# Kernel optimization log

Measured on AMD Instinct MI355X. Metric: run time of the kernel, lower is better.

The kernel has to match this reference:

```python
import jax, jax.numpy as jnp
import numpy as np

N_HEAD, D_MODEL, D_K, D_V = 16, 1024, 64, 64
B, S = 2, 2048
LN_EPS = 1e-5


def setup_inputs() -> dict:
    key = jax.random.key(0)
    ks = jax.random.split(key, 9)
    std_qk = np.sqrt(2.0 / (D_MODEL + D_K)).astype(np.float32)
    std_v = np.sqrt(2.0 / (D_MODEL + D_V)).astype(np.float32)
    return {
        "q": jax.random.normal(ks[0], (B, S, D_MODEL), jnp.float32),
        "k": jax.random.normal(ks[1], (B, S, D_MODEL), jnp.float32),
        "v": jax.random.normal(ks[2], (B, S, D_MODEL), jnp.float32),
        # nn.Linear weights stored as [out, in]; we apply x @ W.T
        "w_qs": jax.random.normal(ks[3], (N_HEAD * D_K, D_MODEL), jnp.float32) * std_qk,
        "w_ks": jax.random.normal(ks[4], (N_HEAD * D_K, D_MODEL), jnp.float32) * std_qk,
        "w_vs": jax.random.normal(ks[5], (N_HEAD * D_V, D_MODEL), jnp.float32) * std_v,
        "fc_w": jax.random.normal(ks[6], (D_MODEL, N_HEAD * D_V), jnp.float32) * np.sqrt(2.0 / (D_MODEL + N_HEAD * D_V)).astype(np.float32),
        "fc_b": jnp.zeros((D_MODEL,), jnp.float32),
        "ln_g": jnp.ones((D_MODEL,), jnp.float32),
        "ln_b": jnp.zeros((D_MODEL,), jnp.float32),
    }


def reference(q, k, v, w_qs, w_ks, w_vs, fc_w, fc_b, ln_g, ln_b):
    temperature = jnp.asarray(np.power(D_K, 0.5), q.dtype)
    residual = q
    # projections -> [b, s, h, d]
    qh = (q @ w_qs.T).reshape(B, S, N_HEAD, D_K)
    kh = (k @ w_ks.T).reshape(B, S, N_HEAD, D_K)
    vh = (v @ w_vs.T).reshape(B, S, N_HEAD, D_V)
    # scaled dot-product attention (dropout = identity in eval)
    attn = jnp.einsum('bqhd,bkhd->bhqk', qh, kh) / temperature
    attn = jax.nn.softmax(attn, axis=-1)  # (log_softmax in source is unused)
    out = jnp.einsum('bhqk,bkhd->bqhd', attn, vh).reshape(B, S, N_HEAD * D_V)
    out = out @ fc_w.T + fc_b
    # layer norm over last dim
    x = out + residual
    mu = jnp.mean(x, axis=-1, keepdims=True)
    var = jnp.var(x, axis=-1, keepdims=True)
    return (x - mu) * jax.lax.rsqrt(var + LN_EPS) * ln_g + ln_b
```

## Files before the change

kernel.cpp:

```cpp
#include <hip/hip_runtime.h>
#include <hip/hip_bf16.h>

typedef _Float16 f16x8 __attribute__((ext_vector_type(8)));
typedef _Float16 f16x4 __attribute__((ext_vector_type(4)));
typedef _Float16 f16x2 __attribute__((ext_vector_type(2)));
typedef float f32x4 __attribute__((ext_vector_type(4)));

#define DEVI __device__ __forceinline__

constexpr int S_LEN = 2048;
constexpr int DM    = 1024;
constexpr int NH    = 16;
constexpr int DHD   = 64;
constexpr int MTOT  = 2 * S_LEN;

DEVI f32x4 mfma16(f16x8 a, f16x8 b, f32x4 c) {
    return __builtin_amdgcn_mfma_f32_16x16x32_f16(a, b, c, 0, 0, 0);
}

DEVI f16x2 cvt_pk(float a, float b) {
    return __builtin_bit_cast(f16x2, __builtin_amdgcn_cvt_pkrtz(a, b));
}

__global__ void k_conv(const float* __restrict__ s0, const float* __restrict__ s1,
                       const float* __restrict__ s2, const float* __restrict__ s3,
                       const float* __restrict__ s4, const float* __restrict__ s5,
                       const float* __restrict__ s6,
                       _Float16* __restrict__ d0, _Float16* __restrict__ d1,
                       _Float16* __restrict__ d2, _Float16* __restrict__ d3,
                       _Float16* __restrict__ d4, _Float16* __restrict__ d5,
                       _Float16* __restrict__ d6)
{
    const int QN4 = (MTOT * DM) / 4;
    const int WN4 = (DM * DM) / 4;
    const int TOT = 3 * QN4 + 4 * WN4;
    int stride = gridDim.x * blockDim.x;
    for (int i = blockIdx.x * blockDim.x + threadIdx.x; i < TOT; i += stride) {
        const float* s; _Float16* d; int off;
        if (i < 3 * QN4) {
            int t = i / QN4; off = i - t * QN4;
            s = t == 0 ? s0 : (t == 1 ? s1 : s2);
            d = t == 0 ? d0 : (t == 1 ? d1 : d2);
        } else {
            int j = i - 3 * QN4;
            int t = j / WN4; off = j - t * WN4;
            s = t == 0 ? s3 : (t == 1 ? s4 : (t == 2 ? s5 : s6));
            d = t == 0 ? d3 : (t == 1 ? d4 : (t == 2 ? d5 : d6));
        }
        float4 v = reinterpret_cast<const float4*>(s)[off];
        f16x4 o;
        o[0] = (_Float16)v.x; o[1] = (_Float16)v.y;
        o[2] = (_Float16)v.z; o[3] = (_Float16)v.w;
        *reinterpret_cast<f16x4*>(d + (size_t)off * 4) = o;
    }
}

DEVI void gemm_main(const _Float16* __restrict__ A, const _Float16* __restrict__ Bw,
                    int K, int m0, int n0,
                    _Float16* As, _Float16* Bs, f32x4 (&acc)[4][4])
{
    const int tid = threadIdx.x;
    const int lane = tid & 63;
    const int w = tid >> 6;
    const int wm = w >> 1, wn = w & 1;
    const int lrow = lane & 15, lg = lane >> 4;
    const int srow = lane >> 3;
    const int sslot = lane & 7;

#pragma unroll
    for (int i = 0; i < 4; i++)
#pragma unroll
        for (int j = 0; j < 4; j++) acc[i][j] = f32x4{0.f, 0.f, 0.f, 0.f};

    f16x8 ra[4], rb[4];
#pragma unroll
    for (int q = 0; q < 4; q++) {
        int row = w * 8 + srow + q * 32;
        ra[q] = *reinterpret_cast<const f16x8*>(A  + (size_t)(m0 + row) * K + sslot * 8);
        rb[q] = *reinterpret_cast<const f16x8*>(Bw + (size_t)(n0 + row) * K + sslot * 8);
    }

    const int kTiles = K >> 6;
    for (int kt = 0; kt < kTiles; ++kt) {
        __syncthreads();
#pragma unroll
        for (int q = 0; q < 4; q++) {
            int row = w * 8 + srow + q * 32;
            int slot = sslot ^ (row & 7);
            *reinterpret_cast<f16x8*>(As + row * 64 + slot * 8) = ra[q];
            *reinterpret_cast<f16x8*>(Bs + row * 64 + slot * 8) = rb[q];
        }
        __syncthreads();
        if (kt + 1 < kTiles) {
#pragma unroll
            for (int q = 0; q < 4; q++) {
                int row = w * 8 + srow + q * 32;
                ra[q] = *reinterpret_cast<const f16x8*>(A  + (size_t)(m0 + row) * K + (kt + 1) * 64 + sslot * 8);
                rb[q] = *reinterpret_cast<const f16x8*>(Bw + (size_t)(n0 + row) * K + (kt + 1) * 64 + sslot * 8);
            }
        }
#pragma unroll
        for (int kk = 0; kk < 2; kk++) {
            f16x8 af[4], bfm[4];
#pragma unroll
            for (int i = 0; i < 4; i++) {
                int row = wm * 64 + i * 16 + lrow;
                int slot = (kk * 4 + lg) ^ (row & 7);
                af[i] = *reinterpret_cast<const f16x8*>(As + row * 64 + slot * 8);
            }
#pragma unroll
            for (int j = 0; j < 4; j++) {
                int row = wn * 64 + j * 16 + lrow;
                int slot = (kk * 4 + lg) ^ (row & 7);
                bfm[j] = *reinterpret_cast<const f16x8*>(Bs + row * 64 + slot * 8);
            }
#pragma unroll
            for (int i = 0; i < 4; i++)
#pragma unroll
                for (int j = 0; j < 4; j++)
                    acc[i][j] = mfma16(af[i], bfm[j], acc[i][j]);
        }
    }
}

__global__ __launch_bounds__(256, 2)
void k_proj(const _Float16* __restrict__ qb, const _Float16* __restrict__ kb,
            const _Float16* __restrict__ vb,
            const _Float16* __restrict__ wq, const _Float16* __restrict__ wk,
            const _Float16* __restrict__ wv,
            _Float16* __restrict__ Qh, _Float16* __restrict__ Kh, _Float16* __restrict__ Vt)
{
    __shared__ __align__(16) _Float16 As[128 * 64];
    __shared__ __align__(16) _Float16 Bs[128 * 64];
    const int z = blockIdx.z;
    const _Float16* A = z == 0 ? qb : (z == 1 ? kb : vb);
    const _Float16* B = z == 0 ? wq : (z == 1 ? wk : wv);
    const int m0 = blockIdx.x * 128, n0 = blockIdx.y * 128;
    f32x4 acc[4][4];
    gemm_main(A, B, DM, m0, n0, As, Bs, acc);

    const int lane = threadIdx.x & 63, w = threadIdx.x >> 6;
    const int wm = w >> 1, wn = w & 1;
    const int lrow = lane & 15, lg = lane >> 4;

    if (z < 2) {
        _Float16* O = z == 0 ? Qh : Kh;
        const float scale = (z == 0) ? 0.18033688011112042f : 1.0f;
#pragma unroll
        for (int i = 0; i < 4; i++)
#pragma unroll
            for (int j = 0; j < 4; j++) {
                int n = n0 + wn * 64 + j * 16 + lrow;
                int h = n >> 6, d = n & 63;
#pragma unroll
                for (int r = 0; r < 4; r++) {
                    int m = m0 + wm * 64 + i * 16 + lg * 4 + r;
                    int b = m >> 11, s = m & (S_LEN - 1);
                    size_t idx = ((size_t)(b * NH + h) * S_LEN + s) * DHD + d;
                    O[idx] = (_Float16)(acc[i][j][r] * scale);
                }
            }
    } else {
#pragma unroll
        for (int i = 0; i < 4; i++) {
            int m = m0 + wm * 64 + i * 16 + lg * 4;
            int b = m >> 11, s = m & (S_LEN - 1);
#pragma unroll
            for (int j = 0; j < 4; j++) {
                int n = n0 + wn * 64 + j * 16 + lrow;
                int h = n >> 6, d = n & 63;
                size_t idx = ((size_t)(b * NH + h) * DHD + d) * S_LEN + s;
                f16x4 pk;
#pragma unroll
                for (int r = 0; r < 4; r++) pk[r] = (_Float16)acc[i][j][r];
                *reinterpret_cast<f16x4*>(Vt + idx) = pk;
            }
        }
    }
}

__global__ __launch_bounds__(256, 4)
void k_attn(const _Float16* __restrict__ Q, const _Float16* __restrict__ Kh,
            const _Float16* __restrict__ Vt, _Float16* __restrict__ Ob)
{
    __shared__ __align__(16) _Float16 Kl[2][64 * 64];
    __shared__ __align__(16) _Float16 Vl[2][64 * 64];
    __shared__ __align__(16) _Float16 Pl[4][16 * 64];

    const int tid  = threadIdx.x;
    const int lane = tid & 63, w = tid >> 6;
    const int lrow = lane & 15, lg = lane >> 4;

    const int raw  = blockIdx.x;
    const int swz  = (raw & 7) * 128 + (raw >> 3);
    const int bh   = swz >> 5;
    const int qblk = swz & 31;
    const int q0   = qblk * 64 + w * 16;

    const _Float16* Qb = Q  + (size_t)bh * S_LEN * DHD;
    const _Float16* Kb = Kh + (size_t)bh * S_LEN * DHD;
    const _Float16* Vb = Vt + (size_t)bh * DHD * S_LEN;

    f16x8 qf[2];
#pragma unroll
    for (int ks = 0; ks < 2; ks++)
        qf[ks] = *reinterpret_cast<const f16x8*>(Qb + (size_t)(q0 + lrow) * DHD + ks * 32 + lg * 8);

    f32x4 oacc[4];
#pragma unroll
    for (int df = 0; df < 4; df++) oacc[df] = f32x4{0.f, 0.f, 0.f, 0.f};
    float lsum = 0.f;

    const int srow8 = lane >> 3, sslot = lane & 7;
    const _Float16* gK = Kb + (size_t)(w * 16 + srow8) * DHD   + sslot * 8;
    const _Float16* gV = Vb + (size_t)(w * 16 + srow8) * S_LEN + sslot * 8;
    const int lds_st = (w * 16 + srow8) * 64 + (sslot ^ srow8) * 8;

    f16x8 stK[2], stV[2];
#pragma unroll
    for (int i = 0; i < 2; i++) {
        stK[i] = *reinterpret_cast<const f16x8*>(gK + i * 8 * DHD);
        stV[i] = *reinterpret_cast<const f16x8*>(gV + i * 8 * S_LEN);
    }

    for (int t = 0; t < 32; ++t) {
        const int cur = t & 1;
        _Float16* Kc = Kl[cur];
        _Float16* Vc = Vl[cur];
#pragma unroll
        for (int i = 0; i < 2; i++) {
            *reinterpret_cast<f16x8*>(Kc + lds_st + i * 8 * 64) = stK[i];
            *reinterpret_cast<f16x8*>(Vc + lds_st + i * 8 * 64) = stV[i];
        }
        if (t + 1 < 32) {
#pragma unroll
            for (int i = 0; i < 2; i++) {
                stK[i] = *reinterpret_cast<const f16x8*>(gK + (size_t)(t + 1) * 64 * DHD + i * 8 * DHD);
                stV[i] = *reinterpret_cast<const f16x8*>(gV + (t + 1) * 64 + i * 8 * S_LEN);
            }
        }
        asm volatile("s_waitcnt lgkmcnt(0)" ::: "memory");
        __builtin_amdgcn_s_barrier();

#pragma unroll
        for (int kf = 0; kf < 4; kf++) {
            const int r = kf * 16 + lrow;
            f16x8 k0 = *reinterpret_cast<const f16x8*>(Kc + r * 64 + ((lg    ) ^ (r & 7)) * 8);
            f16x8 k1 = *reinterpret_cast<const f16x8*>(Kc + r * 64 + ((4 + lg) ^ (r & 7)) * 8);
            __builtin_amdgcn_s_setprio(1);
            f32x4 sc = mfma16(k0, qf[0], f32x4{0.f, 0.f, 0.f, 0.f});
            sc = mfma16(k1, qf[1], sc);
            __builtin_amdgcn_s_setprio(0);
            float p0 = exp2f(sc[0] - 7.f), p1 = exp2f(sc[1] - 7.f);
            float p2 = exp2f(sc[2] - 7.f), p3 = exp2f(sc[3] - 7.f);
            lsum += (p0 + p1) + (p2 + p3);
            f16x2 h01 = cvt_pk(p0, p1);
            f16x2 h23 = cvt_pk(p2, p3);
            const int sl = (kf * 2 + (lg >> 1)) ^ (lrow & 7);
            _Float16* pp = &Pl[w][lrow * 64 + sl * 8 + (lg & 1) * 4];
            *reinterpret_cast<f16x2*>(pp)     = h01;
            *reinterpret_cast<f16x2*>(pp + 2) = h23;
        }

#pragma unroll
        for (int ks = 0; ks < 2; ks++) {
            f16x8 pa = *reinterpret_cast<const f16x8*>(
                &Pl[w][lrow * 64 + ((ks * 4 + lg) ^ (lrow & 7)) * 8]);
            __builtin_amdgcn_s_setprio(1);
#pragma unroll
            for (int df = 0; df < 4; df++) {
                const int r = df * 16 + lrow;
                f16x8 vf = *reinterpret_cast<const f16x8*>(Vc + r * 64 + ((ks * 4 + lg) ^ (r & 7)) * 8);
                oacc[df] = mfma16(pa, vf, oacc[df]);
            }
            __builtin_amdgcn_s_setprio(0);
        }
    }

    lsum += __shfl_xor(lsum, 16);
    lsum += __shfl_xor(lsum, 32);
    const float inv = 1.0f / lsum;
    const int b = bh >> 4, h = bh & 15;
#pragma unroll
    for (int r = 0; r < 4; r++) {
        const float iq = __shfl(inv, lg * 4 + r);
        const int m = b * S_LEN + q0 + lg * 4 + r;
#pragma unroll
        for (int df = 0; df < 4; df++)
            Ob[(size_t)m * DM + h * 64 + df * 16 + lrow] = (_Float16)(oacc[df][r] * iq);
    }
}

__global__ __launch_bounds__(256, 2)
void k_fc(const _Float16* __restrict__ Ob, const _Float16* __restrict__ Wfc,
          const float* __restrict__ bias, float* __restrict__ out)
{
    __shared__ __align__(16) _Float16 As[128 * 64];
    __shared__ __align__(16) _Float16 Bs[128 * 64];
    const int m0 = blockIdx.x * 128, n0 = blockIdx.y * 128;
    f32x4 acc[4][4];
    gemm_main(Ob, Wfc, DM, m0, n0, As, Bs, acc);

    const int lane = threadIdx.x & 63, w = threadIdx.x >> 6;
    const int wm = w >> 1, wn = w & 1;
    const int lrow = lane & 15, lg = lane >> 4;
#pragma unroll
    for (int j = 0; j < 4; j++) {
        int n = n0 + wn * 64 + j * 16 + lrow;
        float bv = bias[n];
#pragma unroll
        for (int i = 0; i < 4; i++)
#pragma unroll
            for (int r = 0; r < 4; r++) {
                int m = m0 + wm * 64 + i * 16 + lg * 4 + r;
                out[(size_t)m * DM + n] = acc[i][j][r] + bv;
            }
    }
}

__global__ void k_ln(const float* __restrict__ x, const float* __restrict__ res,
                     const float* __restrict__ g, const float* __restrict__ be,
                     float* __restrict__ out)
{
    int row = blockIdx.x * 4 + (threadIdx.x >> 6);
    int lane = threadIdx.x & 63;
    const float4* xr = reinterpret_cast<const float4*>(x + (size_t)row * DM);
    const float4* rr = reinterpret_cast<const float4*>(res + (size_t)row * DM);
    float4 v[4];
    float sum = 0.f, sq = 0.f;
#pragma unroll
    for (int t = 0; t < 4; t++) {
        float4 a = xr[lane + 64 * t];
        float4 b = rr[lane + 64 * t];
        float4 c = make_float4(a.x + b.x, a.y + b.y, a.z + b.z, a.w + b.w);
        v[t] = c;
        sum += c.x + c.y + c.z + c.w;
        sq  += c.x * c.x + c.y * c.y + c.z * c.z + c.w * c.w;
    }
#pragma unroll
    for (int o = 1; o < 64; o <<= 1) { sum += __shfl_xor(sum, o); sq += __shfl_xor(sq, o); }
    float mu = sum * (1.f / DM);
    float rstd = rsqrtf(fmaxf(sq * (1.f / DM) - mu * mu, 0.f) + 1e-5f);
    float4* orow = reinterpret_cast<float4*>(out + (size_t)row * DM);
    const float4* gr = reinterpret_cast<const float4*>(g);
    const float4* br = reinterpret_cast<const float4*>(be);
#pragma unroll
    for (int t = 0; t < 4; t++) {
        float4 gg = gr[lane + 64 * t], bb = br[lane + 64 * t];
        float4 c = v[t];
        orow[lane + 64 * t] = make_float4((c.x - mu) * rstd * gg.x + bb.x,
                                          (c.y - mu) * rstd * gg.y + bb.y,
                                          (c.z - mu) * rstd * gg.z + bb.z,
                                          (c.w - mu) * rstd * gg.w + bb.w);
    }
}

extern "C" void kernel_launch(void* const* d_in, const int* in_sizes, int n_in,
                              void* d_out, int out_size, void* d_ws, size_t ws_size,
                              hipStream_t stream)
{
    const float* q    = (const float*)d_in[0];
    const float* k    = (const float*)d_in[1];
    const float* v    = (const float*)d_in[2];
    const float* w_qs = (const float*)d_in[3];
    const float* w_ks = (const float*)d_in[4];
    const float* w_vs = (const float*)d_in[5];
    const float* fc_w = (const float*)d_in[6];
    const float* fc_b = (const float*)d_in[7];
    const float* ln_g = (const float*)d_in[8];
    const float* ln_b = (const float*)d_in[9];
    float* out = (float*)d_out;

    if (ws_size < (size_t)67108864) return;

    _Float16* ws  = (_Float16*)d_ws;
    _Float16* qbf = ws;
    _Float16* kbf = qbf + 4194304;
    _Float16* vbf = kbf + 4194304;
    _Float16* wq  = vbf + 4194304;
    _Float16* wk  = wq + 1048576;
    _Float16* wv  = wk + 1048576;
    _Float16* wfc = wv + 1048576;
    _Float16* Qh  = wfc + 1048576;
    _Float16* Kh  = Qh + 4194304;
    _Float16* Vt  = Kh + 4194304;
    _Float16* Ob  = Vt + 4194304;
    float* fco = (float*)d_ws;

    k_conv<<<2048, 256, 0, stream>>>(q, k, v, w_qs, w_ks, w_vs, fc_w,
                                     qbf, kbf, vbf, wq, wk, wv, wfc);
    k_proj<<<dim3(32, 8, 3), 256, 0, stream>>>(qbf, kbf, vbf, wq, wk, wv, Qh, Kh, Vt);
    k_attn<<<1024, 256, 0, stream>>>(Qh, Kh, Vt, Ob);
    k_fc<<<dim3(32, 8), 256, 0, stream>>>(Ob, wfc, fc_b, fco);
    k_ln<<<1024, 256, 0, stream>>>(fco, q, ln_g, ln_b, out);
}
```

Before: 151.2 us.

## Split-K the output projection, emit fp16 partials, and fold softmax sums into MFMA

The fc GEMM is split into two K-halves across a third grid dimension, doubling the block count from 256 to 512 so more CUs are busy. Each half writes fp16 partial outputs, which the layernorm kernel sums together with the residual. In the attention kernel, the -7 offset is folded into the MFMA accumulator init and exp2 uses the hardware builtin. The row sums are now computed by an extra MFMA against a ones vector instead of scalar adds and shuffles, and P stores are merged into one 4-wide write. The cost is fp16 rounding of the fc outputs and an extra partial-sum read in layernorm.

```diff
diff --git a/kernel.cpp b/kernel.cpp
--- a/kernel.cpp
+++ b/kernel.cpp
@@ -20,6 +20,14 @@
 
 DEVI f16x2 cvt_pk(float a, float b) {
     return __builtin_bit_cast(f16x2, __builtin_amdgcn_cvt_pkrtz(a, b));
+}
+
+DEVI float fexp2(float x) {
+#if __has_builtin(__builtin_amdgcn_exp2f)
+    return __builtin_amdgcn_exp2f(x);
+#else
+    return exp2f(x);
+#endif
 }
 
 __global__ void k_conv(const float* __restrict__ s0, const float* __restrict__ s1,
@@ -56,7 +64,7 @@
 }
 
 DEVI void gemm_main(const _Float16* __restrict__ A, const _Float16* __restrict__ Bw,
-                    int K, int m0, int n0,
+                    int kLen, int ld, int m0, int n0,
                     _Float16* As, _Float16* Bs, f32x4 (&acc)[4][4])
 {
     const int tid = threadIdx.x;
@@ -76,11 +84,11 @@
 #pragma unroll
     for (int q = 0; q < 4; q++) {
         int row = w * 8 + srow + q * 32;
-        ra[q] = *reinterpret_cast<const f16x8*>(A  + (size_t)(m0 + row) * K + sslot * 8);
-        rb[q] = *reinterpret_cast<const f16x8*>(Bw + (size_t)(n0 + row) * K + sslot * 8);
-    }
-
-    const int kTiles = K >> 6;
+        ra[q] = *reinterpret_cast<const f16x8*>(A  + (size_t)(m0 + row) * ld + sslot * 8);
+        rb[q] = *reinterpret_cast<const f16x8*>(Bw + (size_t)(n0 + row) * ld + sslot * 8);
+    }
+
+    const int kTiles = kLen >> 6;
     for (int kt = 0; kt < kTiles; ++kt) {
         __syncthreads();
 #pragma unroll
@@ -95,8 +103,8 @@
 #pragma unroll
             for (int q = 0; q < 4; q++) {
                 int row = w * 8 + srow + q * 32;
-                ra[q] = *reinterpret_cast<const f16x8*>(A  + (size_t)(m0 + row) * K + (kt + 1) * 64 + sslot * 8);
-                rb[q] = *reinterpret_cast<const f16x8*>(Bw + (size_t)(n0 + row) * K + (kt + 1) * 64 + sslot * 8);
+                ra[q] = *reinterpret_cast<const f16x8*>(A  + (size_t)(m0 + row) * ld + (kt + 1) * 64 + sslot * 8);
+                rb[q] = *reinterpret_cast<const f16x8*>(Bw + (size_t)(n0 + row) * ld + (kt + 1) * 64 + sslot * 8);
             }
         }
 #pragma unroll
@@ -137,7 +145,7 @@
     const _Float16* B = z == 0 ? wq : (z == 1 ? wk : wv);
     const int m0 = blockIdx.x * 128, n0 = blockIdx.y * 128;
     f32x4 acc[4][4];
-    gemm_main(A, B, DM, m0, n0, As, Bs, acc);
+    gemm_main(A, B, DM, DM, m0, n0, As, Bs, acc);
 
     const int lane = threadIdx.x & 63, w = threadIdx.x >> 6;
     const int wm = w >> 1, wn = w & 1;
@@ -209,7 +217,11 @@
     f32x4 oacc[4];
 #pragma unroll
     for (int df = 0; df < 4; df++) oacc[df] = f32x4{0.f, 0.f, 0.f, 0.f};
-    float lsum = 0.f;
+    f32x4 lacc = f32x4{0.f, 0.f, 0.f, 0.f};
+
+    f16x8 vones;
+#pragma unroll
+    for (int i = 0; i < 8; i++) vones[i] = (_Float16)1.0f;
 
     const int srow8 = lane >> 3, sslot = lane & 7;
     const _Float16* gK = Kb + (size_t)(w * 16 + srow8) * DHD   + sslot * 8;
@@ -248,18 +260,14 @@
             f16x8 k0 = *reinterpret_cast<const f16x8*>(Kc + r * 64 + ((lg    ) ^ (r & 7)) * 8);
             f16x8 k1 = *reinterpret_cast<const f16x8*>(Kc + r * 64 + ((4 + lg) ^ (r & 7)) * 8);
             __builtin_amdgcn_s_setprio(1);
-            f32x4 sc = mfma16(k0, qf[0], f32x4{0.f, 0.f, 0.f, 0.f});
+            f32x4 sc = mfma16(k0, qf[0], f32x4{-7.f, -7.f, -7.f, -7.f});
             sc = mfma16(k1, qf[1], sc);
             __builtin_amdgcn_s_setprio(0);
-            float p0 = exp2f(sc[0] - 7.f), p1 = exp2f(sc[1] - 7.f);
-            float p2 = exp2f(sc[2] - 7.f), p3 = exp2f(sc[3] - 7.f);
-            lsum += (p0 + p1) + (p2 + p3);
-            f16x2 h01 = cvt_pk(p0, p1);
-            f16x2 h23 = cvt_pk(p2, p3);
+            float p0 = fexp2(sc[0]), p1 = fexp2(sc[1]);
+            float p2 = fexp2(sc[2]), p3 = fexp2(sc[3]);
+            f16x4 hh = __builtin_shufflevector(cvt_pk(p0, p1), cvt_pk(p2, p3), 0, 1, 2, 3);
             const int sl = (kf * 2 + (lg >> 1)) ^ (lrow & 7);
-            _Float16* pp = &Pl[w][lrow * 64 + sl * 8 + (lg & 1) * 4];
-            *reinterpret_cast<f16x2*>(pp)     = h01;
-            *reinterpret_cast<f16x2*>(pp + 2) = h23;
+            *reinterpret_cast<f16x4*>(&Pl[w][lrow * 64 + sl * 8 + (lg & 1) * 4]) = hh;
         }
 
 #pragma unroll
@@ -273,17 +281,15 @@
                 f16x8 vf = *reinterpret_cast<const f16x8*>(Vc + r * 64 + ((ks * 4 + lg) ^ (r & 7)) * 8);
                 oacc[df] = mfma16(pa, vf, oacc[df]);
             }
+            lacc = mfma16(pa, vones, lacc);
             __builtin_amdgcn_s_setprio(0);
         }
     }
 
-    lsum += __shfl_xor(lsum, 16);
-    lsum += __shfl_xor(lsum, 32);
-    const float inv = 1.0f / lsum;
     const int b = bh >> 4, h = bh & 15;
 #pragma unroll
     for (int r = 0; r < 4; r++) {
-        const float iq = __shfl(inv, lg * 4 + r);
+        const float iq = 1.0f / lacc[r];
         const int m = b * S_LEN + q0 + lg * 4 + r;
 #pragma unroll
         for (int df = 0; df < 4; df++)
@@ -293,46 +299,55 @@
 
 __global__ __launch_bounds__(256, 2)
 void k_fc(const _Float16* __restrict__ Ob, const _Float16* __restrict__ Wfc,
-          const float* __restrict__ bias, float* __restrict__ out)
+          const float* __restrict__ bias,
+          _Float16* __restrict__ fcoA, _Float16* __restrict__ fcoB)
 {
     __shared__ __align__(16) _Float16 As[128 * 64];
     __shared__ __align__(16) _Float16 Bs[128 * 64];
+    const int z = blockIdx.z;
     const int m0 = blockIdx.x * 128, n0 = blockIdx.y * 128;
     f32x4 acc[4][4];
-    gemm_main(Ob, Wfc, DM, m0, n0, As, Bs, acc);
-
+    gemm_main(Ob + z * 512, Wfc + z * 512, 512, DM, m0, n0, As, Bs, acc);
+
+    _Float16* out = z == 0 ? fcoA : fcoB;
     const int lane = threadIdx.x & 63, w = threadIdx.x >> 6;
     const int wm = w >> 1, wn = w & 1;
     const int lrow = lane & 15, lg = lane >> 4;
 #pragma unroll
     for (int j = 0; j < 4; j++) {
         int n = n0 + wn * 64 + j * 16 + lrow;
-        float bv = bias[n];
+        float bv = (z == 0) ? bias[n] : 0.f;
 #pragma unroll
         for (int i = 0; i < 4; i++)
 #pragma unroll
             for (int r = 0; r < 4; r++) {
                 int m = m0 + wm * 64 + i * 16 + lg * 4 + r;
-                out[(size_t)m * DM + n] = acc[i][j][r] + bv;
-            }
-    }
-}
-
-__global__ void k_ln(const float* __restrict__ x, const float* __restrict__ res,
+                out[(size_t)m * DM + n] = (_Float16)(acc[i][j][r] + bv);
+            }
+    }
+}
+
+__global__ void k_ln(const _Float16* __restrict__ fa, const _Float16* __restrict__ fb,
+                     const float* __restrict__ res,
                      const float* __restrict__ g, const float* __restrict__ be,
                      float* __restrict__ out)
 {
     int row = blockIdx.x * 4 + (threadIdx.x >> 6);
     int lane = threadIdx.x & 63;
-    const float4* xr = reinterpret_cast<const float4*>(x + (size_t)row * DM);
+    const f16x4* ar = reinterpret_cast<const f16x4*>(fa + (size_t)row * DM);
+    const f16x4* br2 = reinterpret_cast<const f16x4*>(fb + (size_t)row * DM);
     const float4* rr = reinterpret_cast<const float4*>(res + (size_t)row * DM);
     float4 v[4];
     float sum = 0.f, sq = 0.f;
 #pragma unroll
     for (int t = 0; t < 4; t++) {
-        float4 a = xr[lane + 64 * t];
+        f16x4 a = ar[lane + 64 * t];
+        f16x4 bq = br2[lane + 64 * t];
         float4 b = rr[lane + 64 * t];
-        float4 c = make_float4(a.x + b.x, a.y + b.y, a.z + b.z, a.w + b.w);
+        float4 c = make_float4((float)a[0] + (float)bq[0] + b.x,
+                               (float)a[1] + (float)bq[1] + b.y,
+                               (float)a[2] + (float)bq[2] + b.z,
+                               (float)a[3] + (float)bq[3] + b.w);
         v[t] = c;
         sum += c.x + c.y + c.z + c.w;
         sq  += c.x * c.x + c.y * c.y + c.z * c.z + c.w * c.w;
@@ -343,10 +358,10 @@
     float rstd = rsqrtf(fmaxf(sq * (1.f / DM) - mu * mu, 0.f) + 1e-5f);
     float4* orow = reinterpret_cast<float4*>(out + (size_t)row * DM);
     const float4* gr = reinterpret_cast<const float4*>(g);
-    const float4* br = reinterpret_cast<const float4*>(be);
+    const float4* brr = reinterpret_cast<const float4*>(be);
 #pragma unroll
     for (int t = 0; t < 4; t++) {
-        float4 gg = gr[lane + 64 * t], bb = br[lane + 64 * t];
+        float4 gg = gr[lane + 64 * t], bb = brr[lane + 64 * t];
         float4 c = v[t];
         orow[lane + 64 * t] = make_float4((c.x - mu) * rstd * gg.x + bb.x,
                                           (c.y - mu) * rstd * gg.y + bb.y,
@@ -385,12 +400,13 @@
     _Float16* Kh  = Qh + 4194304;
     _Float16* Vt  = Kh + 4194304;
     _Float16* Ob  = Vt + 4194304;
-    float* fco = (float*)d_ws;
+    _Float16* fcoA = qbf;
+    _Float16* fcoB = kbf;
 
     k_conv<<<2048, 256, 0, stream>>>(q, k, v, w_qs, w_ks, w_vs, fc_w,
                                      qbf, kbf, vbf, wq, wk, wv, wfc);
     k_proj<<<dim3(32, 8, 3), 256, 0, stream>>>(qbf, kbf, vbf, wq, wk, wv, Qh, Kh, Vt);
     k_attn<<<1024, 256, 0, stream>>>(Qh, Kh, Vt, Ob);
-    k_fc<<<dim3(32, 8), 256, 0, stream>>>(Ob, wfc, fc_b, fco);
-    k_ln<<<1024, 256, 0, stream>>>(fco, q, ln_g, ln_b, out);
-}
+    k_fc<<<dim3(32, 8, 2), 256, 0, stream>>>(Ob, wfc, fc_b, fcoA, fcoB);
+    k_ln<<<1024, 256, 0, stream>>>(fcoA, fcoB, q, ln_g, ln_b, out);
+}
```

Result: faster. 134.1 us (-11.3%).
